# Kernel optimization log

Hardware: AMD Instinct MI355X
Metric: run time of the kernel (lower is better)

The kernel has to match this reference:

```python
import jax, jax.numpy as jnp
import numpy as np

IGNORE_INDEX = -100
W_HARD = 0.5
W_SOFT = 0.5
TEMP = 1.0
BT, H, V = 2048, 4096, 32000


def setup_inputs() -> dict:
    key = jax.random.key(0)
    k1, k2, k3, k4, k5 = jax.random.split(key, 5)
    student = jax.random.normal(k1, (BT, H // 2), dtype=jnp.float32)
    teacher = jax.random.normal(k2, (BT, H), dtype=jnp.float32)
    target = jax.random.randint(k3, (BT,), 0, V)
    # Linear weights are [out_features, in_features] like nn.Linear
    student_weight = jax.random.normal(k4, (V, H // 2), dtype=jnp.float32) * 0.02
    teacher_weight = jax.random.normal(k5, (V, H), dtype=jnp.float32) * 0.02
    return {
        "student": student,
        "teacher": teacher,
        "target": target,
        "student_weight": student_weight,
        "teacher_weight": teacher_weight,
    }


def reference(student, teacher, target, student_weight, teacher_weight):
    # project to vocab logits: [BT, V]
    s_logits = (student @ student_weight.T) / TEMP
    t_logits = (teacher @ teacher_weight.T) / TEMP

    valid = target != IGNORE_INDEX
    n_valid = valid.sum().astype(s_logits.dtype)

    # hard loss: cross-entropy summed over valid tokens / n_valid
    logp = jax.nn.log_softmax(s_logits, axis=-1)
    safe_tgt = jnp.where(valid, target, 0)
    nll = -jnp.take_along_axis(logp, safe_tgt[:, None], axis=-1)[:, 0]
    hard_loss = jnp.where(valid, nll, 0.0).sum() / n_valid

    # soft loss: 1 - cosine similarity of row-normalized logits, sum / n_valid
    s_norm = s_logits * jax.lax.rsqrt((s_logits * s_logits).sum(-1, keepdims=True) + 1e-12)
    t_norm = t_logits * jax.lax.rsqrt((t_logits * t_logits).sum(-1, keepdims=True) + 1e-12)
    cos_sim = (s_norm * t_norm).sum(-1)  # [BT]
    soft_loss = (1.0 - cos_sim).sum() / n_valid

    return W_HARD * hard_loss + W_SOFT * soft_loss
```

## Files before the change

### kernel.cpp

```cpp
#include <hip/hip_runtime.h>
#include <hip/hip_bf16.h>
#include <stdint.h>

#define BT 2048
#define HS 2048
#define HT 4096
#define NVOCAB 32000
#define IGN (-100)

typedef unsigned short u16;
typedef __attribute__((ext_vector_type(4))) float f32x4;
typedef __attribute__((ext_vector_type(8))) short short8;
typedef __attribute__((ext_vector_type(2))) unsigned int u32x2;
typedef __attribute__((ext_vector_type(4))) unsigned int u32x4;

__device__ inline unsigned int pack2_bf16(float a, float b) {
  union { __hip_bfloat162 h; unsigned int u; } cv;
  cv.h = __float22bfloat162_rn(make_float2(a, b));
  return cv.u;
}

__device__ inline void async16(const void* g, void* l) {
  __builtin_amdgcn_global_load_lds(
      (const __attribute__((address_space(1))) void*)g,
      (__attribute__((address_space(3))) void*)l, 16, 0, 0);
}

__global__ void cvt_f32_bf16(const float4* __restrict__ in, u32x2* __restrict__ out, int n4) {
  int i = blockIdx.x * blockDim.x + threadIdx.x;
  if (i >= n4) return;
  float4 v = in[i];
  u32x2 o;
  o.x = pack2_bf16(v.x, v.y);
  o.y = pack2_bf16(v.z, v.w);
  out[i] = o;
}

template <bool WB16>
__device__ inline void gemm_nt(const u16* __restrict__ A, int lda,
                               const void* __restrict__ Bv, int ldb, int K,
                               u16* stA, u16* stB, f32x4 (&acc)[4][4]) {
  const int tid = threadIdx.x;
  const int lane = tid & 63;
  const int w = tid >> 6;
  const int wr = w >> 1, wc = w & 1;
  const int q = lane >> 4, l15 = lane & 15;

  const u16* aPtr0 = A + (size_t)(w * 32 + (lane >> 2)) * lda + ((lane & 3) * 8);
  const u16* aPtr1 = aPtr0 + (size_t)16 * lda;
  u16* ldsA0 = stA + (size_t)(w * 2) * 512;
  u16* ldsA1 = stA + (size_t)(w * 2 + 1) * 512;

  const u16* Bb = (const u16*)Bv;
  const u16* bPtr0 = Bb + (size_t)(w * 32 + (lane >> 2)) * ldb + ((lane & 3) * 8);
  const u16* bPtr1 = bPtr0 + (size_t)16 * ldb;
  u16* ldsB0 = stB + (size_t)(w * 2) * 512;
  u16* ldsB1 = stB + (size_t)(w * 2 + 1) * 512;

  const float* Bf = (const float*)Bv;
  const float* bPtrF = Bf + (size_t)(tid >> 1) * ldb + (tid & 1) * 16;
  u16* ldsBw = stB + (tid >> 1) * 32 + (tid & 1) * 16;

  for (int k0 = 0; k0 < K; k0 += 32) {
    __syncthreads();
    async16(aPtr0 + k0, ldsA0);
    async16(aPtr1 + k0, ldsA1);
    if constexpr (WB16) {
      async16(bPtr0 + k0, ldsB0);
      async16(bPtr1 + k0, ldsB1);
    } else {
      const float4* bp = (const float4*)(bPtrF + k0);
      float4 f0 = bp[0], f1 = bp[1], f2 = bp[2], f3 = bp[3];
      u32x4 w0, w1;
      w0.x = pack2_bf16(f0.x, f0.y); w0.y = pack2_bf16(f0.z, f0.w);
      w0.z = pack2_bf16(f1.x, f1.y); w0.w = pack2_bf16(f1.z, f1.w);
      w1.x = pack2_bf16(f2.x, f2.y); w1.y = pack2_bf16(f2.z, f2.w);
      w1.z = pack2_bf16(f3.x, f3.y); w1.w = pack2_bf16(f3.z, f3.w);
      ((u32x4*)ldsBw)[0] = w0;
      ((u32x4*)ldsBw)[1] = w1;
    }
    __syncthreads();

    short8 af[4], bf[4];
#pragma unroll
    for (int f = 0; f < 4; f++)
      af[f] = *(const short8*)&stA[(wr * 64 + f * 16 + l15) * 32 + q * 8];
#pragma unroll
    for (int f = 0; f < 4; f++)
      bf[f] = *(const short8*)&stB[(wc * 64 + f * 16 + l15) * 32 + q * 8];
#pragma unroll
    for (int i = 0; i < 4; i++)
#pragma unroll
      for (int j = 0; j < 4; j++)
        acc[i][j] = __builtin_amdgcn_mfma_f32_16x16x32_bf16(af[i], bf[j], acc[i][j], 0, 0, 0);
  }
}

template <bool WB16>
__global__ __launch_bounds__(256) void kmain(
    const u16* __restrict__ sAb, const u16* __restrict__ tAb,
    const void* __restrict__ sW, const void* __restrict__ tW,
    const int* __restrict__ target,
    float* __restrict__ pe, float* __restrict__ ps,
    float* __restrict__ pt, float* __restrict__ pd,
    float* __restrict__ tgtLogit) {
  __shared__ u16 stA[128 * 32];
  __shared__ u16 stB[128 * 32];
  __shared__ u16 sStore[128 * 132];
  __shared__ int tgtLds[128];

  const int bid = blockIdx.x;
  const int cb = bid >> 4;
  const int rb = bid & 15;
  const int row0 = rb * 128;
  const int col0 = cb * 128;

  const int tid = threadIdx.x;
  const int lane = tid & 63;
  const int w = tid >> 6;
  const int wr = w >> 1, wc = w & 1;
  const int l15 = lane & 15;
  const int q4 = (lane >> 4) << 2;

  if (tid < 128) tgtLds[tid] = target[row0 + tid];

  f32x4 acc[4][4];
#pragma unroll
  for (int i = 0; i < 4; i++)
#pragma unroll
    for (int j = 0; j < 4; j++) acc[i][j] = (f32x4){0.f, 0.f, 0.f, 0.f};

  {
    const char* bBase;
    if constexpr (WB16)
      bBase = (const char*)sW + (size_t)col0 * HS * sizeof(u16);
    else
      bBase = (const char*)sW + (size_t)col0 * HS * sizeof(float);
    gemm_nt<WB16>(sAb + (size_t)row0 * HS, HS, (const void*)bBase, HS, HS, stA, stB, acc);
  }

#pragma unroll
  for (int fr = 0; fr < 4; fr++) {
    const int r0 = wr * 64 + fr * 16 + q4;
    float se[4] = {0.f, 0.f, 0.f, 0.f}, sq[4] = {0.f, 0.f, 0.f, 0.f};
#pragma unroll
    for (int fc = 0; fc < 4; fc++) {
      f32x4 v = acc[fr][fc];
      const int cLoc = wc * 64 + fc * 16 + l15;
      const int cGlob = col0 + cLoc;
      u32x2 pk;
      pk.x = pack2_bf16(v[0], v[1]);
      pk.y = pack2_bf16(v[2], v[3]);
      *(u32x2*)&sStore[cLoc * 132 + r0] = pk;
#pragma unroll
      for (int rg = 0; rg < 4; rg++) {
        float x = v[rg];
        se[rg] += __expf(x);
        sq[rg] += x * x;
        if (tgtLds[r0 + rg] == cGlob) tgtLogit[row0 + r0 + rg] = x;
      }
    }
#pragma unroll
    for (int m = 1; m < 16; m <<= 1) {
#pragma unroll
      for (int rg = 0; rg < 4; rg++) {
        se[rg] += __shfl_xor(se[rg], m, 64);
        sq[rg] += __shfl_xor(sq[rg], m, 64);
      }
    }
    if (l15 == 0) {
      size_t pbase = (size_t)(cb * 2 + wc) * BT + row0 + r0;
#pragma unroll
      for (int rg = 0; rg < 4; rg++) {
        pe[pbase + rg] = se[rg];
        ps[pbase + rg] = sq[rg];
      }
    }
  }

#pragma unroll
  for (int i = 0; i < 4; i++)
#pragma unroll
    for (int j = 0; j < 4; j++) acc[i][j] = (f32x4){0.f, 0.f, 0.f, 0.f};
  {
    const char* bBase;
    if constexpr (WB16)
      bBase = (const char*)tW + (size_t)col0 * HT * sizeof(u16);
    else
      bBase = (const char*)tW + (size_t)col0 * HT * sizeof(float);
    gemm_nt<WB16>(tAb + (size_t)row0 * HT, HT, (const void*)bBase, HT, HT, stA, stB, acc);
  }

#pragma unroll
  for (int fr = 0; fr < 4; fr++) {
    const int r0 = wr * 64 + fr * 16 + q4;
    float st[4] = {0.f, 0.f, 0.f, 0.f}, dt[4] = {0.f, 0.f, 0.f, 0.f};
#pragma unroll
    for (int fc = 0; fc < 4; fc++) {
      f32x4 v = acc[fr][fc];
      const int cLoc = wc * 64 + fc * 16 + l15;
      u32x2 p = *(const u32x2*)&sStore[cLoc * 132 + r0];
      float sv[4];
      sv[0] = __uint_as_float(p.x << 16);
      sv[1] = __uint_as_float(p.x & 0xffff0000u);
      sv[2] = __uint_as_float(p.y << 16);
      sv[3] = __uint_as_float(p.y & 0xffff0000u);
#pragma unroll
      for (int rg = 0; rg < 4; rg++) {
        float t = v[rg];
        st[rg] += t * t;
        dt[rg] += sv[rg] * t;
      }
    }
#pragma unroll
    for (int m = 1; m < 16; m <<= 1) {
#pragma unroll
      for (int rg = 0; rg < 4; rg++) {
        st[rg] += __shfl_xor(st[rg], m, 64);
        dt[rg] += __shfl_xor(dt[rg], m, 64);
      }
    }
    if (l15 == 0) {
      size_t pbase = (size_t)(cb * 2 + wc) * BT + row0 + r0;
#pragma unroll
      for (int rg = 0; rg < 4; rg++) {
        pt[pbase + rg] = st[rg];
        pd[pbase + rg] = dt[rg];
      }
    }
  }
}

__global__ void kreduce(const float* __restrict__ pe, const float* __restrict__ ps,
                        const float* __restrict__ pt, const float* __restrict__ pd,
                        const float* __restrict__ tgtLogit, const int* __restrict__ target,
                        float* __restrict__ scal) {
  int row = blockIdx.x * blockDim.x + threadIdx.x;
  float se = 0.f, ss = 0.f, st = 0.f, dt = 0.f;
  for (int j = 0; j < 500; j++) {
    int idx = j * BT + row;
    se += pe[idx];
    ss += ps[idx];
    st += pt[idx];
    dt += pd[idx];
  }
  int tgt = target[row];
  bool valid = (tgt != IGN);
  float hard = valid ? (__logf(se) - tgtLogit[row]) : 0.f;
  float cosv = dt * rsqrtf(ss + 1e-12f) * rsqrtf(st + 1e-12f);
  float soft = 1.f - cosv;
  float nv = valid ? 1.f : 0.f;
  for (int m = 1; m < 64; m <<= 1) {
    hard += __shfl_xor(hard, m, 64);
    soft += __shfl_xor(soft, m, 64);
    nv += __shfl_xor(nv, m, 64);
  }
  if ((threadIdx.x & 63) == 0) {
    atomicAdd(&scal[0], hard);
    atomicAdd(&scal[1], soft);
    atomicAdd(&scal[2], nv);
  }
}

__global__ void kfinal(const float* __restrict__ scal, float* __restrict__ out) {
  float nv = scal[2];
  out[0] = 0.5f * scal[0] / nv + 0.5f * scal[1] / nv;
}

extern "C" void kernel_launch(void* const* d_in, const int* in_sizes, int n_in,
                              void* d_out, int out_size, void* d_ws, size_t ws_size,
                              hipStream_t stream) {
  const float* student = (const float*)d_in[0];
  const float* teacher = (const float*)d_in[1];
  const int* target = (const int*)d_in[2];
  const float* sW = (const float*)d_in[3];
  const float* tW = (const float*)d_in[4];
  float* out = (float*)d_out;

  char* ws = (char*)d_ws;

  const size_t NEED = 434774028;

  if (ws_size >= NEED) {
    u16* sAb = (u16*)(ws);
    u16* tAb = (u16*)(ws + 8388608);
    u16* sWb = (u16*)(ws + 25165824);
    u16* tWb = (u16*)(ws + 156237824);
    float* pe = (float*)(ws + 418381824);
    float* ps = (float*)(ws + 422477824);
    float* pt = (float*)(ws + 426573824);
    float* pd = (float*)(ws + 430669824);
    float* tgtLogit = (float*)(ws + 434765824);
    float* scal = (float*)(ws + 434774016);

    hipMemsetAsync(scal, 0, 3 * sizeof(float), stream);

    {
      int n4 = BT * HS / 4;
      cvt_f32_bf16<<<(n4 + 255) / 256, 256, 0, stream>>>((const float4*)student, (u32x2*)sAb, n4);
    }
    {
      int n4 = BT * HT / 4;
      cvt_f32_bf16<<<(n4 + 255) / 256, 256, 0, stream>>>((const float4*)teacher, (u32x2*)tAb, n4);
    }
    {
      int n4 = NVOCAB * HS / 4;
      cvt_f32_bf16<<<(n4 + 255) / 256, 256, 0, stream>>>((const float4*)sW, (u32x2*)sWb, n4);
    }
    {
      int n4 = NVOCAB * HT / 4;
      cvt_f32_bf16<<<(n4 + 255) / 256, 256, 0, stream>>>((const float4*)tW, (u32x2*)tWb, n4);
    }

    kmain<true><<<dim3(4000), dim3(256), 0, stream>>>(
        sAb, tAb, (const void*)sWb, (const void*)tWb, target, pe, ps, pt, pd, tgtLogit);
    kreduce<<<dim3(8), dim3(256), 0, stream>>>(pe, ps, pt, pd, tgtLogit, target, scal);
    kfinal<<<dim3(1), dim3(1), 0, stream>>>(scal, out);
  } else {
    u16* sAb = (u16*)(ws);
    u16* tAb = (u16*)(ws + 8388608);
    float* pe = (float*)(ws + 25165824);
    float* ps = (float*)(ws + 25165824 + 4096000);
    float* pt = (float*)(ws + 25165824 + 8192000);
    float* pd = (float*)(ws + 25165824 + 12288000);
    float* tgtLogit = (float*)(ws + 41549824);
    float* scal = (float*)(ws + 41558016);

    hipMemsetAsync(scal, 0, 3 * sizeof(float), stream);

    {
      int n4 = BT * HS / 4;
      cvt_f32_bf16<<<(n4 + 255) / 256, 256, 0, stream>>>((const float4*)student, (u32x2*)sAb, n4);
    }
    {
      int n4 = BT * HT / 4;
      cvt_f32_bf16<<<(n4 + 255) / 256, 256, 0, stream>>>((const float4*)teacher, (u32x2*)tAb, n4);
    }

    kmain<false><<<dim3(4000), dim3(256), 0, stream>>>(
        sAb, tAb, (const void*)sW, (const void*)tW, target, pe, ps, pt, pd, tgtLogit);
    kreduce<<<dim3(8), dim3(256), 0, stream>>>(pe, ps, pt, pd, tgtLogit, target, scal);
    kfinal<<<dim3(1), dim3(1), 0, stream>>>(scal, out);
  }
}
```

Before: 2.174 ms.

## Rewrite fused GEMM with 256x256 tiles, 4-stage async LDS pipeline, split reduction

```diff
diff --git a/kernel.cpp b/kernel.cpp
--- a/kernel.cpp
+++ b/kernel.cpp
@@ -8,14 +8,19 @@
 #define NVOCAB 32000
 #define IGN (-100)
 
+#define NTS (HS / 32)
+#define NTT (HT / 32)
+#define TOT (NTS + NTT)
+
 typedef unsigned short u16;
+typedef unsigned int u32;
 typedef __attribute__((ext_vector_type(4))) float f32x4;
 typedef __attribute__((ext_vector_type(8))) short short8;
 typedef __attribute__((ext_vector_type(2))) unsigned int u32x2;
 typedef __attribute__((ext_vector_type(4))) unsigned int u32x4;
 
-__device__ inline unsigned int pack2_bf16(float a, float b) {
-  union { __hip_bfloat162 h; unsigned int u; } cv;
+__device__ inline u32 pack2_bf16(float a, float b) {
+  union { __hip_bfloat162 h; u32 u; } cv;
   cv.h = __float22bfloat162_rn(make_float2(a, b));
   return cv.u;
 }
@@ -26,185 +31,184 @@
       (__attribute__((address_space(3))) void*)l, 16, 0, 0);
 }
 
-__global__ void cvt_f32_bf16(const float4* __restrict__ in, u32x2* __restrict__ out, int n4) {
+__global__ void cvt_f32_bf16(const float4* __restrict__ in, u32x4* __restrict__ out, int n8) {
   int i = blockIdx.x * blockDim.x + threadIdx.x;
-  if (i >= n4) return;
-  float4 v = in[i];
-  u32x2 o;
-  o.x = pack2_bf16(v.x, v.y);
-  o.y = pack2_bf16(v.z, v.w);
+  if (i >= n8) return;
+  float4 a = in[2 * i], b = in[2 * i + 1];
+  u32x4 o;
+  o.x = pack2_bf16(a.x, a.y);
+  o.y = pack2_bf16(a.z, a.w);
+  o.z = pack2_bf16(b.x, b.y);
+  o.w = pack2_bf16(b.z, b.w);
   out[i] = o;
 }
 
-template <bool WB16>
-__device__ inline void gemm_nt(const u16* __restrict__ A, int lda,
-                               const void* __restrict__ Bv, int ldb, int K,
-                               u16* stA, u16* stB, f32x4 (&acc)[4][4]) {
-  const int tid = threadIdx.x;
-  const int lane = tid & 63;
-  const int w = tid >> 6;
-  const int wr = w >> 1, wc = w & 1;
-  const int q = lane >> 4, l15 = lane & 15;
-
-  const u16* aPtr0 = A + (size_t)(w * 32 + (lane >> 2)) * lda + ((lane & 3) * 8);
-  const u16* aPtr1 = aPtr0 + (size_t)16 * lda;
-  u16* ldsA0 = stA + (size_t)(w * 2) * 512;
-  u16* ldsA1 = stA + (size_t)(w * 2 + 1) * 512;
-
-  const u16* Bb = (const u16*)Bv;
-  const u16* bPtr0 = Bb + (size_t)(w * 32 + (lane >> 2)) * ldb + ((lane & 3) * 8);
-  const u16* bPtr1 = bPtr0 + (size_t)16 * ldb;
-  u16* ldsB0 = stB + (size_t)(w * 2) * 512;
-  u16* ldsB1 = stB + (size_t)(w * 2 + 1) * 512;
-
-  const float* Bf = (const float*)Bv;
-  const float* bPtrF = Bf + (size_t)(tid >> 1) * ldb + (tid & 1) * 16;
-  u16* ldsBw = stB + (tid >> 1) * 32 + (tid & 1) * 16;
-
-  for (int k0 = 0; k0 < K; k0 += 32) {
-    __syncthreads();
-    async16(aPtr0 + k0, ldsA0);
-    async16(aPtr1 + k0, ldsA1);
-    if constexpr (WB16) {
-      async16(bPtr0 + k0, ldsB0);
-      async16(bPtr1 + k0, ldsB1);
-    } else {
-      const float4* bp = (const float4*)(bPtrF + k0);
-      float4 f0 = bp[0], f1 = bp[1], f2 = bp[2], f3 = bp[3];
-      u32x4 w0, w1;
-      w0.x = pack2_bf16(f0.x, f0.y); w0.y = pack2_bf16(f0.z, f0.w);
-      w0.z = pack2_bf16(f1.x, f1.y); w0.w = pack2_bf16(f1.z, f1.w);
-      w1.x = pack2_bf16(f2.x, f2.y); w1.y = pack2_bf16(f2.z, f2.w);
-      w1.z = pack2_bf16(f3.x, f3.y); w1.w = pack2_bf16(f3.z, f3.w);
-      ((u32x4*)ldsBw)[0] = w0;
-      ((u32x4*)ldsBw)[1] = w1;
-    }
-    __syncthreads();
-
-    short8 af[4], bf[4];
-#pragma unroll
-    for (int f = 0; f < 4; f++)
-      af[f] = *(const short8*)&stA[(wr * 64 + f * 16 + l15) * 32 + q * 8];
-#pragma unroll
-    for (int f = 0; f < 4; f++)
-      bf[f] = *(const short8*)&stB[(wc * 64 + f * 16 + l15) * 32 + q * 8];
-#pragma unroll
-    for (int i = 0; i < 4; i++)
-#pragma unroll
-      for (int j = 0; j < 4; j++)
-        acc[i][j] = __builtin_amdgcn_mfma_f32_16x16x32_bf16(af[i], bf[j], acc[i][j], 0, 0, 0);
-  }
-}
-
-template <bool WB16>
-__global__ __launch_bounds__(256) void kmain(
+__global__ __launch_bounds__(512, 2) void kmain(
     const u16* __restrict__ sAb, const u16* __restrict__ tAb,
-    const void* __restrict__ sW, const void* __restrict__ tW,
+    const u16* __restrict__ sWb, const u16* __restrict__ tWb,
     const int* __restrict__ target,
     float* __restrict__ pe, float* __restrict__ ps,
     float* __restrict__ pt, float* __restrict__ pd,
     float* __restrict__ tgtLogit) {
-  __shared__ u16 stA[128 * 32];
-  __shared__ u16 stB[128 * 32];
-  __shared__ u16 sStore[128 * 132];
-  __shared__ int tgtLds[128];
+  __shared__ u16 lds[4][2][8192];
+  __shared__ int tgtLds[256];
 
   const int bid = blockIdx.x;
-  const int cb = bid >> 4;
-  const int rb = bid & 15;
-  const int row0 = rb * 128;
-  const int col0 = cb * 128;
+  const int wgid = (bid & 7) * 125 + (bid >> 3);
+  const int rb = wgid / 125;
+  const int cb = wgid % 125;
+  const int row0 = rb * 256;
+  const int col0 = cb * 256;
 
   const int tid = threadIdx.x;
   const int lane = tid & 63;
   const int w = tid >> 6;
-  const int wr = w >> 1, wc = w & 1;
+  const int wr = w >> 2;
+  const int wc = w & 3;
   const int l15 = lane & 15;
-  const int q4 = (lane >> 4) << 2;
-
-  if (tid < 128) tgtLds[tid] = target[row0 + tid];
-
-  f32x4 acc[4][4];
-#pragma unroll
-  for (int i = 0; i < 4; i++)
-#pragma unroll
-    for (int j = 0; j < 4; j++) acc[i][j] = (f32x4){0.f, 0.f, 0.f, 0.f};
-
-  {
-    const char* bBase;
-    if constexpr (WB16)
-      bBase = (const char*)sW + (size_t)col0 * HS * sizeof(u16);
-    else
-      bBase = (const char*)sW + (size_t)col0 * HS * sizeof(float);
-    gemm_nt<WB16>(sAb + (size_t)row0 * HS, HS, (const void*)bBase, HS, HS, stA, stB, acc);
-  }
-
-#pragma unroll
-  for (int fr = 0; fr < 4; fr++) {
-    const int r0 = wr * 64 + fr * 16 + q4;
-    float se[4] = {0.f, 0.f, 0.f, 0.f}, sq[4] = {0.f, 0.f, 0.f, 0.f};
-#pragma unroll
-    for (int fc = 0; fc < 4; fc++) {
-      f32x4 v = acc[fr][fc];
-      const int cLoc = wc * 64 + fc * 16 + l15;
-      const int cGlob = col0 + cLoc;
-      u32x2 pk;
-      pk.x = pack2_bf16(v[0], v[1]);
-      pk.y = pack2_bf16(v[2], v[3]);
-      *(u32x2*)&sStore[cLoc * 132 + r0] = pk;
-#pragma unroll
-      for (int rg = 0; rg < 4; rg++) {
-        float x = v[rg];
-        se[rg] += __expf(x);
-        sq[rg] += x * x;
-        if (tgtLds[r0 + rg] == cGlob) tgtLogit[row0 + r0 + rg] = x;
+  const int q = lane >> 4;
+  const int q4 = q << 2;
+  const int qp8 = ((q ^ ((l15 >> 1) & 3)) << 3);
+
+  if (tid < 256) tgtLds[tid] = target[row0 + tid];
+
+  const int rowA = w * 32 + (lane >> 2);
+  const int gp8 = (((lane & 3) ^ ((lane >> 3) & 3)) << 3);
+  const u32 offS = (u32)rowA * HS + gp8;
+  const u32 offT = (u32)rowA * HT + gp8;
+  const u16* baseAs = sAb + (size_t)row0 * HS;
+  const u16* baseAt = tAb + (size_t)row0 * HT;
+  const u16* baseBs = sWb + (size_t)col0 * HS;
+  const u16* baseBt = tWb + (size_t)col0 * HT;
+  const int wdst = w * 1024;
+
+  f32x4 acc[8][4];
+#pragma unroll
+  for (int m = 0; m < 8; m++)
+#pragma unroll
+    for (int n = 0; n < 4; n++) acc[m][n] = (f32x4){0.f, 0.f, 0.f, 0.f};
+  u32 stash[8][4][2];
+
+#pragma unroll
+  for (int t = 0; t < 3; t++) {
+    const u16* pA = baseAs + offS + t * 32;
+    async16(pA, &lds[t][0][wdst]);
+    async16(pA + 16 * HS, &lds[t][0][wdst + 512]);
+    const u16* pB = baseBs + offS + t * 32;
+    async16(pB, &lds[t][1][wdst]);
+    async16(pB + 16 * HS, &lds[t][1][wdst + 512]);
+  }
+  asm volatile("s_waitcnt lgkmcnt(0)" ::: "memory");
+  __builtin_amdgcn_s_barrier();
+  __builtin_amdgcn_sched_barrier(0);
+
+  for (int T = 0; T < TOT; T++) {
+    const int slot = T & 3;
+    const int slotP = (T + 3) & 3;
+    const int Tp = (T + 3 < TOT) ? T + 3 : TOT - 1;
+    const u16 *bA, *bB;
+    u32 off;
+    int ld16, k0;
+    if (Tp < NTS) { bA = baseAs; bB = baseBs; off = offS; ld16 = 16 * HS; k0 = Tp * 32; }
+    else          { bA = baseAt; bB = baseBt; off = offT; ld16 = 16 * HT; k0 = (Tp - NTS) * 32; }
+
+    asm volatile("s_waitcnt vmcnt(8)" ::: "memory");
+    __builtin_amdgcn_s_barrier();
+    __builtin_amdgcn_sched_barrier(0);
+
+    const u16* sA = &lds[slot][0][0];
+    const u16* sB = &lds[slot][1][0];
+
+    short8 bf[4], af[4];
+#pragma unroll
+    for (int n = 0; n < 4; n++)
+      bf[n] = *(const short8*)&sB[(wc * 64 + n * 16 + l15) * 32 + qp8];
+#pragma unroll
+    for (int m = 0; m < 4; m++)
+      af[m] = *(const short8*)&sA[(wr * 128 + m * 16 + l15) * 32 + qp8];
+    {
+      const u16* p = bA + off + k0;
+      async16(p, &lds[slotP][0][wdst]);
+      async16(p + ld16, &lds[slotP][0][wdst + 512]);
+    }
+    __builtin_amdgcn_s_setprio(1);
+#pragma unroll
+    for (int m = 0; m < 4; m++)
+#pragma unroll
+      for (int n = 0; n < 4; n++)
+        acc[m][n] = __builtin_amdgcn_mfma_f32_16x16x32_bf16(af[m], bf[n], acc[m][n], 0, 0, 0);
+    __builtin_amdgcn_s_setprio(0);
+    __builtin_amdgcn_s_barrier();
+    __builtin_amdgcn_sched_barrier(0);
+
+#pragma unroll
+    for (int m = 0; m < 4; m++)
+      af[m] = *(const short8*)&sA[(wr * 128 + (m + 4) * 16 + l15) * 32 + qp8];
+    {
+      const u16* p = bB + off + k0;
+      async16(p, &lds[slotP][1][wdst]);
+      async16(p + ld16, &lds[slotP][1][wdst + 512]);
+    }
+    __builtin_amdgcn_s_setprio(1);
+#pragma unroll
+    for (int m = 0; m < 4; m++)
+#pragma unroll
+      for (int n = 0; n < 4; n++)
+        acc[m + 4][n] = __builtin_amdgcn_mfma_f32_16x16x32_bf16(af[m], bf[n], acc[m + 4][n], 0, 0, 0);
+    __builtin_amdgcn_s_setprio(0);
+    __builtin_amdgcn_s_barrier();
+    __builtin_amdgcn_sched_barrier(0);
+
+    if (T == NTS - 1) {
+#pragma unroll
+      for (int m = 0; m < 8; m++) {
+        float se[4] = {0.f, 0.f, 0.f, 0.f}, sq[4] = {0.f, 0.f, 0.f, 0.f};
+        const int rloc = wr * 128 + m * 16 + q4;
+#pragma unroll
+        for (int n = 0; n < 4; n++) {
+          f32x4 v = acc[m][n];
+          stash[m][n][0] = pack2_bf16(v[0], v[1]);
+          stash[m][n][1] = pack2_bf16(v[2], v[3]);
+          const int cGlob = col0 + wc * 64 + n * 16 + l15;
+#pragma unroll
+          for (int rg = 0; rg < 4; rg++) {
+            float x = v[rg];
+            se[rg] += __expf(x);
+            sq[rg] += x * x;
+            if (tgtLds[rloc + rg] == cGlob) tgtLogit[row0 + rloc + rg] = x;
+          }
+          acc[m][n] = (f32x4){0.f, 0.f, 0.f, 0.f};
+        }
+#pragma unroll
+        for (int msk = 1; msk < 16; msk <<= 1) {
+#pragma unroll
+          for (int rg = 0; rg < 4; rg++) {
+            se[rg] += __shfl_xor(se[rg], msk, 64);
+            sq[rg] += __shfl_xor(sq[rg], msk, 64);
+          }
+        }
+        if (l15 == 0) {
+          size_t pbase = (size_t)(cb * 4 + wc) * BT + row0 + rloc;
+#pragma unroll
+          for (int rg = 0; rg < 4; rg++) { pe[pbase + rg] = se[rg]; ps[pbase + rg] = sq[rg]; }
+        }
       }
-    }
-#pragma unroll
-    for (int m = 1; m < 16; m <<= 1) {
-#pragma unroll
-      for (int rg = 0; rg < 4; rg++) {
-        se[rg] += __shfl_xor(se[rg], m, 64);
-        sq[rg] += __shfl_xor(sq[rg], m, 64);
-      }
-    }
-    if (l15 == 0) {
-      size_t pbase = (size_t)(cb * 2 + wc) * BT + row0 + r0;
-#pragma unroll
-      for (int rg = 0; rg < 4; rg++) {
-        pe[pbase + rg] = se[rg];
-        ps[pbase + rg] = sq[rg];
-      }
-    }
-  }
-
-#pragma unroll
-  for (int i = 0; i < 4; i++)
-#pragma unroll
-    for (int j = 0; j < 4; j++) acc[i][j] = (f32x4){0.f, 0.f, 0.f, 0.f};
-  {
-    const char* bBase;
-    if constexpr (WB16)
-      bBase = (const char*)tW + (size_t)col0 * HT * sizeof(u16);
-    else
-      bBase = (const char*)tW + (size_t)col0 * HT * sizeof(float);
-    gemm_nt<WB16>(tAb + (size_t)row0 * HT, HT, (const void*)bBase, HT, HT, stA, stB, acc);
-  }
-
-#pragma unroll
-  for (int fr = 0; fr < 4; fr++) {
-    const int r0 = wr * 64 + fr * 16 + q4;
+      asm volatile("s_waitcnt vmcnt(0)" ::: "memory");
+    }
+  }
+
+#pragma unroll
+  for (int m = 0; m < 8; m++) {
     float st[4] = {0.f, 0.f, 0.f, 0.f}, dt[4] = {0.f, 0.f, 0.f, 0.f};
-#pragma unroll
-    for (int fc = 0; fc < 4; fc++) {
-      f32x4 v = acc[fr][fc];
-      const int cLoc = wc * 64 + fc * 16 + l15;
-      u32x2 p = *(const u32x2*)&sStore[cLoc * 132 + r0];
+    const int rloc = wr * 128 + m * 16 + q4;
+#pragma unroll
+    for (int n = 0; n < 4; n++) {
+      f32x4 v = acc[m][n];
       float sv[4];
-      sv[0] = __uint_as_float(p.x << 16);
-      sv[1] = __uint_as_float(p.x & 0xffff0000u);
-      sv[2] = __uint_as_float(p.y << 16);
-      sv[3] = __uint_as_float(p.y & 0xffff0000u);
+      sv[0] = __uint_as_float(stash[m][n][0] << 16);
+      sv[1] = __uint_as_float(stash[m][n][0] & 0xffff0000u);
+      sv[2] = __uint_as_float(stash[m][n][1] << 16);
+      sv[3] = __uint_as_float(stash[m][n][1] & 0xffff0000u);
 #pragma unroll
       for (int rg = 0; rg < 4; rg++) {
         float t = v[rg];
@@ -213,36 +217,49 @@
       }
     }
 #pragma unroll
-    for (int m = 1; m < 16; m <<= 1) {
+    for (int msk = 1; msk < 16; msk <<= 1) {
 #pragma unroll
       for (int rg = 0; rg < 4; rg++) {
-        st[rg] += __shfl_xor(st[rg], m, 64);
-        dt[rg] += __shfl_xor(dt[rg], m, 64);
+        st[rg] += __shfl_xor(st[rg], msk, 64);
+        dt[rg] += __shfl_xor(dt[rg], msk, 64);
       }
     }
     if (l15 == 0) {
-      size_t pbase = (size_t)(cb * 2 + wc) * BT + row0 + r0;
-#pragma unroll
-      for (int rg = 0; rg < 4; rg++) {
-        pt[pbase + rg] = st[rg];
-        pd[pbase + rg] = dt[rg];
-      }
-    }
-  }
-}
-
-__global__ void kreduce(const float* __restrict__ pe, const float* __restrict__ ps,
-                        const float* __restrict__ pt, const float* __restrict__ pd,
-                        const float* __restrict__ tgtLogit, const int* __restrict__ target,
-                        float* __restrict__ scal) {
-  int row = blockIdx.x * blockDim.x + threadIdx.x;
+      size_t pbase = (size_t)(cb * 4 + wc) * BT + row0 + rloc;
+#pragma unroll
+      for (int rg = 0; rg < 4; rg++) { pt[pbase + rg] = st[rg]; pd[pbase + rg] = dt[rg]; }
+    }
+  }
+}
+
+__global__ void kreduce1(const float* __restrict__ pe, const float* __restrict__ ps,
+                         const float* __restrict__ pt, const float* __restrict__ pd,
+                         float* __restrict__ part) {
+  int row = blockIdx.x * 256 + threadIdx.x;
+  int c = blockIdx.y;
+  float a = 0.f, b = 0.f, cc = 0.f, d = 0.f;
+  int j0 = c * 20;
+  for (int j = j0; j < j0 + 20; j++) {
+    int idx = j * BT + row;
+    a += pe[idx]; b += ps[idx]; cc += pt[idx]; d += pd[idx];
+  }
+  int o = c * BT + row;
+  part[o] = a;
+  part[25 * BT + o] = b;
+  part[50 * BT + o] = cc;
+  part[75 * BT + o] = d;
+}
+
+__global__ void kreduce2(const float* __restrict__ part, const float* __restrict__ tgtLogit,
+                         const int* __restrict__ target, float* __restrict__ scal) {
+  int row = blockIdx.x * 256 + threadIdx.x;
   float se = 0.f, ss = 0.f, st = 0.f, dt = 0.f;
-  for (int j = 0; j < 500; j++) {
-    int idx = j * BT + row;
-    se += pe[idx];
-    ss += ps[idx];
-    st += pt[idx];
-    dt += pd[idx];
+  for (int c = 0; c < 25; c++) {
+    int o = c * BT + row;
+    se += part[o];
+    ss += part[25 * BT + o];
+    st += part[50 * BT + o];
+    dt += part[75 * BT + o];
   }
   int tgt = target[row];
   bool valid = (tgt != IGN);
@@ -278,68 +295,40 @@
   float* out = (float*)d_out;
 
   char* ws = (char*)d_ws;
-
-  const size_t NEED = 434774028;
-
-  if (ws_size >= NEED) {
-    u16* sAb = (u16*)(ws);
-    u16* tAb = (u16*)(ws + 8388608);
-    u16* sWb = (u16*)(ws + 25165824);
-    u16* tWb = (u16*)(ws + 156237824);
-    float* pe = (float*)(ws + 418381824);
-    float* ps = (float*)(ws + 422477824);
-    float* pt = (float*)(ws + 426573824);
-    float* pd = (float*)(ws + 430669824);
-    float* tgtLogit = (float*)(ws + 434765824);
-    float* scal = (float*)(ws + 434774016);
-
-    hipMemsetAsync(scal, 0, 3 * sizeof(float), stream);
-
-    {
-      int n4 = BT * HS / 4;
-      cvt_f32_bf16<<<(n4 + 255) / 256, 256, 0, stream>>>((const float4*)student, (u32x2*)sAb, n4);
-    }
-    {
-      int n4 = BT * HT / 4;
-      cvt_f32_bf16<<<(n4 + 255) / 256, 256, 0, stream>>>((const float4*)teacher, (u32x2*)tAb, n4);
-    }
-    {
-      int n4 = NVOCAB * HS / 4;
-      cvt_f32_bf16<<<(n4 + 255) / 256, 256, 0, stream>>>((const float4*)sW, (u32x2*)sWb, n4);
-    }
-    {
-      int n4 = NVOCAB * HT / 4;
-      cvt_f32_bf16<<<(n4 + 255) / 256, 256, 0, stream>>>((const float4*)tW, (u32x2*)tWb, n4);
-    }
-
-    kmain<true><<<dim3(4000), dim3(256), 0, stream>>>(
-        sAb, tAb, (const void*)sWb, (const void*)tWb, target, pe, ps, pt, pd, tgtLogit);
-    kreduce<<<dim3(8), dim3(256), 0, stream>>>(pe, ps, pt, pd, tgtLogit, target, scal);
-    kfinal<<<dim3(1), dim3(1), 0, stream>>>(scal, out);
-  } else {
-    u16* sAb = (u16*)(ws);
-    u16* tAb = (u16*)(ws + 8388608);
-    float* pe = (float*)(ws + 25165824);
-    float* ps = (float*)(ws + 25165824 + 4096000);
-    float* pt = (float*)(ws + 25165824 + 8192000);
-    float* pd = (float*)(ws + 25165824 + 12288000);
-    float* tgtLogit = (float*)(ws + 41549824);
-    float* scal = (float*)(ws + 41558016);
-
-    hipMemsetAsync(scal, 0, 3 * sizeof(float), stream);
-
-    {
-      int n4 = BT * HS / 4;
-      cvt_f32_bf16<<<(n4 + 255) / 256, 256, 0, stream>>>((const float4*)student, (u32x2*)sAb, n4);
-    }
-    {
-      int n4 = BT * HT / 4;
-      cvt_f32_bf16<<<(n4 + 255) / 256, 256, 0, stream>>>((const float4*)teacher, (u32x2*)tAb, n4);
-    }
-
-    kmain<false><<<dim3(4000), dim3(256), 0, stream>>>(
-        sAb, tAb, (const void*)sW, (const void*)tW, target, pe, ps, pt, pd, tgtLogit);
-    kreduce<<<dim3(8), dim3(256), 0, stream>>>(pe, ps, pt, pd, tgtLogit, target, scal);
-    kfinal<<<dim3(1), dim3(1), 0, stream>>>(scal, out);
-  }
-}
+  u16* sAb = (u16*)(ws);
+  u16* tAb = (u16*)(ws + 8388608);
+  u16* sWb = (u16*)(ws + 25165824);
+  u16* tWb = (u16*)(ws + 156237824);
+  float* pe = (float*)(ws + 418381824);
+  float* ps = (float*)(ws + 422477824);
+  float* pt = (float*)(ws + 426573824);
+  float* pd = (float*)(ws + 430669824);
+  float* tgtLogit = (float*)(ws + 434765824);
+  float* scal = (float*)(ws + 434774016);
+  float* part = (float*)(ws);
+
+  hipMemsetAsync(scal, 0, 3 * sizeof(float), stream);
+
+  {
+    int n8 = BT * HS / 8;
+    cvt_f32_bf16<<<(n8 + 255) / 256, 256, 0, stream>>>((const float4*)student, (u32x4*)sAb, n8);
+  }
+  {
+    int n8 = BT * HT / 8;
+    cvt_f32_bf16<<<(n8 + 255) / 256, 256, 0, stream>>>((const float4*)teacher, (u32x4*)tAb, n8);
+  }
+  {
+    int n8 = NVOCAB * HS / 8;
+    cvt_f32_bf16<<<(n8 + 255) / 256, 256, 0, stream>>>((const float4*)sW, (u32x4*)sWb, n8);
+  }
+  {
+    int n8 = NVOCAB * HT / 8;
+    cvt_f32_bf16<<<(n8 + 255) / 256, 256, 0, stream>>>((const float4*)tW, (u32x4*)tWb, n8);
+  }
+
+  kmain<<<dim3(1000), dim3(512), 0, stream>>>(sAb, tAb, sWb, tWb, target,
+                                              pe, ps, pt, pd, tgtLogit);
+  kreduce1<<<dim3(8, 25), dim3(256), 0, stream>>>(pe, ps, pt, pd, part);
+  kreduce2<<<dim3(8), dim3(256), 0, stream>>>(part, tgtLogit, target, scal);
+  kfinal<<<dim3(1), dim3(1), 0, stream>>>(scal, out);
+}
```

Measured after the change: 1.743 ms. 1.25x faster.
